# Kernel tuning notes

Measured on AMD Instinct MI355X. Metric: run time of the kernel, lower is better.

The kernel has to match this reference:

```python
import jax, jax.numpy as jnp
import numpy as np

H = 8
LN_EPS = 1e-5


def _layer_norm(t):
    # LayerNorm over last dim, no affine (elementwise_affine=False, bias=False)
    mu = jnp.mean(t, axis=-1, keepdims=True)
    var = jnp.var(t, axis=-1, keepdims=True)
    return (t - mu) / jnp.sqrt(var + LN_EPS)


def setup_inputs() -> dict:
    key = jax.random.key(0)
    ks = jax.random.split(key, 7)
    B, N, D, K = 2, 8192, 512, 32
    x = jax.random.normal(ks[0], (B, N, D), dtype=jnp.float32)
    idx = jax.random.randint(ks[1], (N, K), 0, N)
    s = 1.0 / np.sqrt(D)  # kaiming-ish init scale for stability
    Wq = jax.random.normal(ks[2], (D, D), dtype=jnp.float32) * s
    Wk = jax.random.normal(ks[3], (D, D), dtype=jnp.float32) * s
    Wv = jax.random.normal(ks[4], (D, D), dtype=jnp.float32) * s
    Wout = jax.random.normal(ks[5], (D, D), dtype=jnp.float32) * s
    bout = jnp.zeros((D,), dtype=jnp.float32)
    return {"x": x, "idx": idx, "Wq": Wq, "Wk": Wk, "Wv": Wv, "Wout": Wout, "bout": bout}


def reference(x, idx, Wq, Wk, Wv, Wout, bout):
    B, N, D = x.shape
    d_k = D // H

    def proj(W):
        # torch Linear: x @ W.T ; reshape to (B, H, N, d_k)
        return (x @ W.T).reshape(B, N, H, d_k).transpose(0, 2, 1, 3)

    Q, K, V = proj(Wq), proj(Wk), proj(Wv)
    # per-head LayerNorm on d_k (all heads identical since no affine params)
    Q = _layer_norm(Q)
    K = _layer_norm(K)

    # grouped (neighborhood) attention: gather K,V at neighbor indices
    Kg = K[:, :, idx]  # (B, H, N, k, d_k)
    Vg = V[:, :, idx]  # (B, H, N, k, d_k)
    scores = jnp.einsum('bhnd,bhnkd->bhnk', Q, Kg) / jnp.sqrt(jnp.asarray(d_k, x.dtype))
    attn = jax.nn.softmax(scores, axis=-1)
    out = jnp.einsum('bhnk,bhnkd->bhnd', attn, Vg)  # (B, H, N, d_k)

    out = out.transpose(0, 2, 1, 3).reshape(B, N, D)
    return out @ Wout.T + bout
```

## Files before the change

### kernel.cpp

```cpp
#include <hip/hip_runtime.h>
#include <hip/hip_bf16.h>
#include <math.h>

#define BB 2
#define NN 8192
#define DD 512
#define HH 8
#define DK 64
#define KNB 32
#define BN (BB*NN)
#define BHN (BB*HH*NN)

typedef __attribute__((ext_vector_type(8))) _Float16 f16x8;
typedef __attribute__((ext_vector_type(2))) _Float16 f16x2;
typedef __attribute__((ext_vector_type(4))) float f32x4;

#if __has_builtin(__builtin_amdgcn_fdot2)
#define HAS_FDOT2 1
#endif

__device__ __forceinline__ unsigned short f2h(float f) {
    return __builtin_bit_cast(unsigned short, (_Float16)f);
}
__device__ __forceinline__ f16x2 u2h2(unsigned u) {
    return __builtin_bit_cast(f16x2, u);
}
__device__ __forceinline__ float h2f_lo(unsigned u) {
    return (float)__builtin_bit_cast(_Float16, (unsigned short)(u & 0xffffu));
}
__device__ __forceinline__ float h2f_hi(unsigned u) {
    return (float)__builtin_bit_cast(_Float16, (unsigned short)(u >> 16));
}
__device__ __forceinline__ float dot2h(unsigned a, unsigned b, float c) {
#ifdef HAS_FDOT2
    return __builtin_amdgcn_fdot2(u2h2(a), u2h2(b), c, false);
#else
    c = fmaf(h2f_lo(a), h2f_lo(b), c);
    return fmaf(h2f_hi(a), h2f_hi(b), c);
#endif
}

__device__ __forceinline__ void gload_lds16(const void* gptr, void* lptr) {
    __builtin_amdgcn_global_load_lds(
        (const __attribute__((address_space(1))) unsigned int*)gptr,
        (__attribute__((address_space(3))) unsigned int*)lptr,
        16, 0, 0);
}

__global__ __launch_bounds__(256) void cvt_all(
    const float* __restrict__ x,
    const float* __restrict__ Wq, const float* __restrict__ Wk,
    const float* __restrict__ Wv, const float* __restrict__ Wo,
    unsigned short* __restrict__ Xb, unsigned short* __restrict__ Wfb,
    unsigned short* __restrict__ Wob)
{
    const int blk = blockIdx.x;
    const float* src;
    unsigned short* dst;
    int off;
    if (blk < 8192) {
        off = (blk * 256 + threadIdx.x) * 4;
        src = x; dst = Xb;
    } else {
        const int e = ((blk - 8192) * 256 + threadIdx.x) * 4;
        const int t = e >> 18;
        off = e & 262143;
        src = (t == 0) ? Wq : (t == 1) ? Wk : (t == 2) ? Wv : Wo;
        dst = (t < 3) ? (Wfb + (size_t)t * 262144) : Wob;
    }
    const float4 v = *(const float4*)(src + off);
    ushort4 u;
    u.x = f2h(v.x); u.y = f2h(v.y); u.z = f2h(v.z); u.w = f2h(v.w);
    *(ushort4*)(dst + off) = u;
}

__global__ __launch_bounds__(256) void gemm_qkv(
    const unsigned short* __restrict__ Xb, const unsigned short* __restrict__ Wfb,
    unsigned short* __restrict__ Qh, unsigned short* __restrict__ Kh,
    unsigned short* __restrict__ Vh)
{
    __shared__ unsigned short Als[2][128 * 32];
    __shared__ unsigned short Bls[2][128 * 32];
    const int tid  = threadIdx.x;
    const int wave = tid >> 6, lane = tid & 63;
    const int wm = wave >> 1, wn = wave & 1;
    const int quad = lane >> 4, r = lane & 15;
    const int p = blockIdx.x;
    const int L = (p & 7) * 192 + (p >> 3);
    const int row0 = (L / 12) * 128;
    const int c0   = (L % 12) * 128;

    f32x4 acc[4][4];
    #pragma unroll
    for (int i = 0; i < 4; ++i)
        #pragma unroll
        for (int j = 0; j < 4; ++j) acc[i][j] = (f32x4)0.f;

    const char* Ab = (const char*)Xb;
    const char* Bb = (const char*)Wfb;

    const int li0 = wave * 1024 + lane * 16;
    const int rr0 = li0 >> 6, off0 = li0 & 63;
    const int li1 = 4096 + li0;
    const int rr1 = li1 >> 6, off1 = li1 & 63;

    {
        gload_lds16(Ab + (size_t)(row0 + rr0) * 1024 + off0, (char*)Als[0] + (wave * 1024));
        gload_lds16(Bb + (size_t)(c0   + rr0) * 1024 + off0, (char*)Bls[0] + (wave * 1024));
        gload_lds16(Ab + (size_t)(row0 + rr1) * 1024 + off1, (char*)Als[0] + (4096 + wave * 1024));
        gload_lds16(Bb + (size_t)(c0   + rr1) * 1024 + off1, (char*)Bls[0] + (4096 + wave * 1024));
    }
    __syncthreads();

    for (int kt = 0; kt < 16; ++kt) {
        const int cur = kt & 1;
        if (kt < 15) {
            const int kb = (kt + 1) * 64;
            gload_lds16(Ab + (size_t)(row0 + rr0) * 1024 + kb + off0, (char*)Als[cur ^ 1] + (wave * 1024));
            gload_lds16(Bb + (size_t)(c0   + rr0) * 1024 + kb + off0, (char*)Bls[cur ^ 1] + (wave * 1024));
            gload_lds16(Ab + (size_t)(row0 + rr1) * 1024 + kb + off1, (char*)Als[cur ^ 1] + (4096 + wave * 1024));
            gload_lds16(Bb + (size_t)(c0   + rr1) * 1024 + kb + off1, (char*)Bls[cur ^ 1] + (4096 + wave * 1024));
        }

        f16x8 af[4], bf[4];
        #pragma unroll
        for (int i = 0; i < 4; ++i)
            af[i] = *(const f16x8*)(&Als[cur][(wm * 64 + i * 16 + r) * 32 + quad * 8]);
        #pragma unroll
        for (int j = 0; j < 4; ++j)
            bf[j] = *(const f16x8*)(&Bls[cur][(wn * 64 + j * 16 + r) * 32 + quad * 8]);
        #pragma unroll
        for (int i = 0; i < 4; ++i)
            #pragma unroll
            for (int j = 0; j < 4; ++j)
                acc[i][j] = __builtin_amdgcn_mfma_f32_16x16x32_f16(af[i], bf[j], acc[i][j], 0, 0, 0);

        __syncthreads();
    }

    const int tensor = c0 >> 9;
    unsigned short* OutH = (tensor == 0) ? Qh : (tensor == 1) ? Kh : Vh;

    float mu[4][4], rs[4][4];
    if (tensor < 2) {
        #pragma unroll
        for (int i = 0; i < 4; ++i) {
            #pragma unroll
            for (int reg = 0; reg < 4; ++reg) {
                float sm = acc[i][0][reg] + acc[i][1][reg] + acc[i][2][reg] + acc[i][3][reg];
                sm += __shfl_xor(sm, 1); sm += __shfl_xor(sm, 2);
                sm += __shfl_xor(sm, 4); sm += __shfl_xor(sm, 8);
                const float muv = sm * (1.f / 64.f);
                float qv = 0.f;
                #pragma unroll
                for (int j = 0; j < 4; ++j) {
                    const float dv = acc[i][j][reg] - muv;
                    qv = fmaf(dv, dv, qv);
                }
                qv += __shfl_xor(qv, 1); qv += __shfl_xor(qv, 2);
                qv += __shfl_xor(qv, 4); qv += __shfl_xor(qv, 8);
                mu[i][reg] = muv;
                rs[i][reg] = rsqrtf(qv * (1.f / 64.f) + 1e-5f);
            }
        }
    }

    #pragma unroll
    for (int i = 0; i < 4; ++i) {
        #pragma unroll
        for (int j = 0; j < 4; ++j) {
            const int cc = (c0 & 511) + wn * 64 + j * 16 + r;
            const int h = cc >> 6, d = cc & 63;
            #pragma unroll
            for (int reg = 0; reg < 4; ++reg) {
                const int row = row0 + wm * 64 + i * 16 + quad * 4 + reg;
                const int b = row >> 13, n = row & 8191;
                float v = acc[i][j][reg];
                if (tensor < 2) v = (v - mu[i][reg]) * rs[i][reg];
                OutH[(((size_t)(b * HH + h) * NN + n) << 6) + d] = f2h(v);
            }
        }
    }
}

__global__ __launch_bounds__(256, 2) void attn(
    const unsigned short* __restrict__ Qh, const unsigned short* __restrict__ Kh,
    const unsigned short* __restrict__ Vh,
    const int* __restrict__ idx, unsigned short* __restrict__ Ob)
{
    const int p = blockIdx.x;
    const int L = ((p & 7) << 12) | (p >> 3);
    const int wave = threadIdx.x >> 6;
    const int wid  = L * 4 + wave;
    const int lane = threadIdx.x & 63;
    const int bh = wid >> 13;
    const int n  = wid & 8191;
    const size_t base = (size_t)bh * NN * DK;

    const int g_all = idx[n * KNB + (lane & 31)];

    const int k    = lane >> 1;
    const int half = lane & 1;
    const int g    = __builtin_amdgcn_ds_bpermute(k * 4, g_all);

    const uint4* q4 = (const uint4*)(Qh + base + ((size_t)n << 6) + half * 32);
    const uint4* k4 = (const uint4*)(Kh + base + ((size_t)g << 6) + half * 32);
    float a0 = 0.f, a1 = 0.f;
    {
        const uint4 qa = q4[0], ka = k4[0];
        a0 = dot2h(qa.x, ka.x, a0); a0 = dot2h(qa.y, ka.y, a0);
        a0 = dot2h(qa.z, ka.z, a0); a0 = dot2h(qa.w, ka.w, a0);
    }
    {
        const uint4 qa = q4[1], ka = k4[1];
        a1 = dot2h(qa.x, ka.x, a1); a1 = dot2h(qa.y, ka.y, a1);
        a1 = dot2h(qa.z, ka.z, a1); a1 = dot2h(qa.w, ka.w, a1);
    }
    {
        const uint4 qa = q4[2], ka = k4[2];
        a0 = dot2h(qa.x, ka.x, a0); a0 = dot2h(qa.y, ka.y, a0);
        a0 = dot2h(qa.z, ka.z, a0); a0 = dot2h(qa.w, ka.w, a0);
    }
    {
        const uint4 qa = q4[3], ka = k4[3];
        a1 = dot2h(qa.x, ka.x, a1); a1 = dot2h(qa.y, ka.y, a1);
        a1 = dot2h(qa.z, ka.z, a1); a1 = dot2h(qa.w, ka.w, a1);
    }
    const float acc = a0 + a1;
    const float s = (acc + __shfl_xor(acc, 1)) * 0.125f;

    const float e = __expf(s);
    float tot = e;
    #pragma unroll
    for (int off = 2; off <= 32; off <<= 1) tot += __shfl_xor(tot, off);
    const float pr = e / tot;

    const unsigned prh = (unsigned)f2h(pr);
    const unsigned pp = prh | (((unsigned)__shfl_xor((int)prh, 2)) << 16);

    const char* Vbytes = (const char*)Vh + (base << 1);
    const int c2 = lane & 31, h2 = lane >> 5;
    float o0 = 0.f, o1 = 0.f;
    #pragma unroll
    for (int j = 0; j < 8; ++j) {
        const int r0 = __builtin_amdgcn_ds_bpermute((h2 * 16 + 2 * j) * 4, g_all);
        const int r1 = __builtin_amdgcn_ds_bpermute((h2 * 16 + 2 * j + 1) * 4, g_all);
        const unsigned vx = *(const unsigned*)(Vbytes + (size_t)(r0 * 128) + c2 * 4);
        const unsigned vy = *(const unsigned*)(Vbytes + (size_t)(r1 * 128) + c2 * 4);
        const unsigned ppj = (unsigned)__builtin_amdgcn_ds_bpermute(h2 * 128 + j * 16, (int)pp);
        const unsigned t0 = __builtin_amdgcn_perm(vx, vy, 0x01000504u);
        const unsigned t1 = __builtin_amdgcn_perm(vx, vy, 0x03020706u);
        o0 = dot2h(t0, ppj, o0);
        o1 = dot2h(t1, ppj, o1);
    }
    o0 += __shfl_xor(o0, 32);
    o1 += __shfl_xor(o1, 32);
    if (lane < 32) {
        const int b = bh >> 3, hh = bh & 7;
        const unsigned ov = (unsigned)f2h(o0) | ((unsigned)f2h(o1) << 16);
        *(unsigned*)(Ob + ((size_t)(b * NN + n)) * DD + hh * DK + 2 * c2) = ov;
    }
}

__global__ __launch_bounds__(256) void gemm_out(
    const unsigned short* __restrict__ Ob, const unsigned short* __restrict__ Wob,
    const float* __restrict__ bout, float* __restrict__ out)
{
    __shared__ unsigned short Als[2][128 * 32];
    __shared__ unsigned short Bls[2][128 * 32];
    const int tid  = threadIdx.x;
    const int wave = tid >> 6, lane = tid & 63;
    const int wm = wave >> 1, wn = wave & 1;
    const int quad = lane >> 4, r = lane & 15;
    const int p = blockIdx.x;
    const int L = (p & 7) * 64 + (p >> 3);
    const int row0 = (L >> 2) * 128;
    const int c0   = (L & 3) * 128;

    f32x4 acc[4][4];
    #pragma unroll
    for (int i = 0; i < 4; ++i)
        #pragma unroll
        for (int j = 0; j < 4; ++j) acc[i][j] = (f32x4)0.f;

    const char* Ab = (const char*)Ob;
    const char* Bb = (const char*)Wob;

    const int li0 = wave * 1024 + lane * 16;
    const int rr0 = li0 >> 6, off0 = li0 & 63;
    const int li1 = 4096 + li0;
    const int rr1 = li1 >> 6, off1 = li1 & 63;

    {
        gload_lds16(Ab + (size_t)(row0 + rr0) * 1024 + off0, (char*)Als[0] + (wave * 1024));
        gload_lds16(Bb + (size_t)(c0   + rr0) * 1024 + off0, (char*)Bls[0] + (wave * 1024));
        gload_lds16(Ab + (size_t)(row0 + rr1) * 1024 + off1, (char*)Als[0] + (4096 + wave * 1024));
        gload_lds16(Bb + (size_t)(c0   + rr1) * 1024 + off1, (char*)Bls[0] + (4096 + wave * 1024));
    }
    __syncthreads();

    for (int kt = 0; kt < 16; ++kt) {
        const int cur = kt & 1;
        if (kt < 15) {
            const int kb = (kt + 1) * 64;
            gload_lds16(Ab + (size_t)(row0 + rr0) * 1024 + kb + off0, (char*)Als[cur ^ 1] + (wave * 1024));
            gload_lds16(Bb + (size_t)(c0   + rr0) * 1024 + kb + off0, (char*)Bls[cur ^ 1] + (wave * 1024));
            gload_lds16(Ab + (size_t)(row0 + rr1) * 1024 + kb + off1, (char*)Als[cur ^ 1] + (4096 + wave * 1024));
            gload_lds16(Bb + (size_t)(c0   + rr1) * 1024 + kb + off1, (char*)Bls[cur ^ 1] + (4096 + wave * 1024));
        }

        f16x8 af[4], bf[4];
        #pragma unroll
        for (int i = 0; i < 4; ++i)
            af[i] = *(const f16x8*)(&Als[cur][(wm * 64 + i * 16 + r) * 32 + quad * 8]);
        #pragma unroll
        for (int j = 0; j < 4; ++j)
            bf[j] = *(const f16x8*)(&Bls[cur][(wn * 64 + j * 16 + r) * 32 + quad * 8]);
        #pragma unroll
        for (int i = 0; i < 4; ++i)
            #pragma unroll
            for (int j = 0; j < 4; ++j)
                acc[i][j] = __builtin_amdgcn_mfma_f32_16x16x32_f16(af[i], bf[j], acc[i][j], 0, 0, 0);

        __syncthreads();
    }

    #pragma unroll
    for (int i = 0; i < 4; ++i) {
        #pragma unroll
        for (int j = 0; j < 4; ++j) {
            const int colg = c0 + wn * 64 + j * 16 + r;
            const float bb = bout[colg];
            #pragma unroll
            for (int reg = 0; reg < 4; ++reg) {
                const int row = row0 + wm * 64 + i * 16 + quad * 4 + reg;
                out[((size_t)row << 9) + colg] = acc[i][j][reg] + bb;
            }
        }
    }
}

extern "C" void kernel_launch(void* const* d_in, const int* in_sizes, int n_in,
                              void* d_out, int out_size, void* d_ws, size_t ws_size,
                              hipStream_t stream)
{
    const float* x    = (const float*)d_in[0];
    const int*   idx  = (const int*)  d_in[1];
    const float* Wq   = (const float*)d_in[2];
    const float* Wk   = (const float*)d_in[3];
    const float* Wv   = (const float*)d_in[4];
    const float* Wout = (const float*)d_in[5];
    const float* bout = (const float*)d_in[6];

    char* ws = (char*)d_ws;
    unsigned short* Qh  = (unsigned short*)(ws);
    unsigned short* Kh  = (unsigned short*)(ws + 16777216);
    unsigned short* Vh  = (unsigned short*)(ws + 33554432);
    unsigned short* Xb  = (unsigned short*)(ws + 50331648);
    unsigned short* Ob  = Xb;
    unsigned short* Wfb = (unsigned short*)(ws + 67108864);
    unsigned short* Wob = (unsigned short*)(ws + 68681728);
    float* out = (float*)d_out;

    cvt_all<<<9216, 256, 0, stream>>>(x, Wq, Wk, Wv, Wout, Xb, Wfb, Wob);

    gemm_qkv<<<1536, 256, 0, stream>>>(Xb, Wfb, Qh, Kh, Vh);

    attn<<<BHN / 4, 256, 0, stream>>>(Qh, Kh, Vh, idx, Ob);

    gemm_out<<<512, 256, 0, stream>>>(Ob, Wob, bout, out);
}
```

Baseline: 221.2 us.

## Fuse fp32-to-fp16 conversion of x into the QKV GEMM A-tile load

Removes the separate conversion pass over x. The QKV GEMM now loads fp32 x tiles into registers, converts them to packed fp16 with cvt_pkrtz, and writes them to LDS after the MFMA work for the current tile. The weight-only conversion kernel remains. This saves a 16 MB fp32 read plus an 8 MB fp16 write and its readback. In exchange, the GEMM reads twice as many A bytes from global memory, and each x row is reread by all 12 column blocks, through cache. Conversion also changes from default rounding to round-toward-zero.

```diff
diff --git a/kernel.cpp b/kernel.cpp
--- a/kernel.cpp
+++ b/kernel.cpp
@@ -40,6 +40,10 @@
 #endif
 }
 
+__device__ __forceinline__ unsigned cvt2h(float lo, float hi) {
+    return __builtin_bit_cast(unsigned, __builtin_amdgcn_cvt_pkrtz(lo, hi));
+}
+
 __device__ __forceinline__ void gload_lds16(const void* gptr, void* lptr) {
     __builtin_amdgcn_global_load_lds(
         (const __attribute__((address_space(1))) unsigned int*)gptr,
@@ -47,27 +51,16 @@
         16, 0, 0);
 }
 
-__global__ __launch_bounds__(256) void cvt_all(
-    const float* __restrict__ x,
+__global__ __launch_bounds__(256) void cvt_w(
     const float* __restrict__ Wq, const float* __restrict__ Wk,
     const float* __restrict__ Wv, const float* __restrict__ Wo,
-    unsigned short* __restrict__ Xb, unsigned short* __restrict__ Wfb,
-    unsigned short* __restrict__ Wob)
-{
-    const int blk = blockIdx.x;
-    const float* src;
-    unsigned short* dst;
-    int off;
-    if (blk < 8192) {
-        off = (blk * 256 + threadIdx.x) * 4;
-        src = x; dst = Xb;
-    } else {
-        const int e = ((blk - 8192) * 256 + threadIdx.x) * 4;
-        const int t = e >> 18;
-        off = e & 262143;
-        src = (t == 0) ? Wq : (t == 1) ? Wk : (t == 2) ? Wv : Wo;
-        dst = (t < 3) ? (Wfb + (size_t)t * 262144) : Wob;
-    }
+    unsigned short* __restrict__ Wfb, unsigned short* __restrict__ Wob)
+{
+    const int e = (blockIdx.x * 256 + threadIdx.x) * 4;
+    const int t = e >> 18;
+    const int off = e & 262143;
+    const float* src = (t == 0) ? Wq : (t == 1) ? Wk : (t == 2) ? Wv : Wo;
+    unsigned short* dst = (t < 3) ? (Wfb + (size_t)t * 262144) : Wob;
     const float4 v = *(const float4*)(src + off);
     ushort4 u;
     u.x = f2h(v.x); u.y = f2h(v.y); u.z = f2h(v.z); u.w = f2h(v.w);
@@ -75,7 +68,7 @@
 }
 
 __global__ __launch_bounds__(256) void gemm_qkv(
-    const unsigned short* __restrict__ Xb, const unsigned short* __restrict__ Wfb,
+    const float* __restrict__ x, const unsigned short* __restrict__ Wfb,
     unsigned short* __restrict__ Qh, unsigned short* __restrict__ Kh,
     unsigned short* __restrict__ Vh)
 {
@@ -96,7 +89,6 @@
         #pragma unroll
         for (int j = 0; j < 4; ++j) acc[i][j] = (f32x4)0.f;
 
-    const char* Ab = (const char*)Xb;
     const char* Bb = (const char*)Wfb;
 
     const int li0 = wave * 1024 + lane * 16;
@@ -104,22 +96,34 @@
     const int li1 = 4096 + li0;
     const int rr1 = li1 >> 6, off1 = li1 & 63;
 
-    {
-        gload_lds16(Ab + (size_t)(row0 + rr0) * 1024 + off0, (char*)Als[0] + (wave * 1024));
-        gload_lds16(Bb + (size_t)(c0   + rr0) * 1024 + off0, (char*)Bls[0] + (wave * 1024));
-        gload_lds16(Ab + (size_t)(row0 + rr1) * 1024 + off1, (char*)Als[0] + (4096 + wave * 1024));
-        gload_lds16(Bb + (size_t)(c0   + rr1) * 1024 + off1, (char*)Bls[0] + (4096 + wave * 1024));
+    const int ar = tid >> 3;
+    const int aq = tid & 7;
+
+    float4 va[4];
+    #pragma unroll
+    for (int i = 0; i < 4; ++i)
+        va[i] = *(const float4*)(x + (size_t)(row0 + i * 32 + ar) * 512 + aq * 4);
+    gload_lds16(Bb + (size_t)(c0 + rr0) * 1024 + off0, (char*)Bls[0] + (wave * 1024));
+    gload_lds16(Bb + (size_t)(c0 + rr1) * 1024 + off1, (char*)Bls[0] + (4096 + wave * 1024));
+    #pragma unroll
+    for (int i = 0; i < 4; ++i) {
+        uint2 u;
+        u.x = cvt2h(va[i].x, va[i].y);
+        u.y = cvt2h(va[i].z, va[i].w);
+        *(uint2*)((char*)Als[0] + (i * 32 + ar) * 64 + aq * 8) = u;
     }
     __syncthreads();
 
     for (int kt = 0; kt < 16; ++kt) {
         const int cur = kt & 1;
         if (kt < 15) {
+            const int ke = (kt + 1) * 32;
+            #pragma unroll
+            for (int i = 0; i < 4; ++i)
+                va[i] = *(const float4*)(x + (size_t)(row0 + i * 32 + ar) * 512 + ke + aq * 4);
             const int kb = (kt + 1) * 64;
-            gload_lds16(Ab + (size_t)(row0 + rr0) * 1024 + kb + off0, (char*)Als[cur ^ 1] + (wave * 1024));
-            gload_lds16(Bb + (size_t)(c0   + rr0) * 1024 + kb + off0, (char*)Bls[cur ^ 1] + (wave * 1024));
-            gload_lds16(Ab + (size_t)(row0 + rr1) * 1024 + kb + off1, (char*)Als[cur ^ 1] + (4096 + wave * 1024));
-            gload_lds16(Bb + (size_t)(c0   + rr1) * 1024 + kb + off1, (char*)Bls[cur ^ 1] + (4096 + wave * 1024));
+            gload_lds16(Bb + (size_t)(c0 + rr0) * 1024 + kb + off0, (char*)Bls[cur ^ 1] + (wave * 1024));
+            gload_lds16(Bb + (size_t)(c0 + rr1) * 1024 + kb + off1, (char*)Bls[cur ^ 1] + (4096 + wave * 1024));
         }
 
         f16x8 af[4], bf[4];
@@ -135,6 +139,15 @@
             for (int j = 0; j < 4; ++j)
                 acc[i][j] = __builtin_amdgcn_mfma_f32_16x16x32_f16(af[i], bf[j], acc[i][j], 0, 0, 0);
 
+        if (kt < 15) {
+            #pragma unroll
+            for (int i = 0; i < 4; ++i) {
+                uint2 u;
+                u.x = cvt2h(va[i].x, va[i].y);
+                u.y = cvt2h(va[i].z, va[i].w);
+                *(uint2*)((char*)Als[cur ^ 1] + (i * 32 + ar) * 64 + aq * 8) = u;
+            }
+        }
         __syncthreads();
     }
 
@@ -356,15 +369,14 @@
     unsigned short* Qh  = (unsigned short*)(ws);
     unsigned short* Kh  = (unsigned short*)(ws + 16777216);
     unsigned short* Vh  = (unsigned short*)(ws + 33554432);
-    unsigned short* Xb  = (unsigned short*)(ws + 50331648);
-    unsigned short* Ob  = Xb;
+    unsigned short* Ob  = (unsigned short*)(ws + 50331648);
     unsigned short* Wfb = (unsigned short*)(ws + 67108864);
     unsigned short* Wob = (unsigned short*)(ws + 68681728);
     float* out = (float*)d_out;
 
-    cvt_all<<<9216, 256, 0, stream>>>(x, Wq, Wk, Wv, Wout, Xb, Wfb, Wob);
-
-    gemm_qkv<<<1536, 256, 0, stream>>>(Xb, Wfb, Qh, Kh, Vh);
+    cvt_w<<<1024, 256, 0, stream>>>(Wq, Wk, Wv, Wout, Wfb, Wob);
+
+    gemm_qkv<<<1536, 256, 0, stream>>>(x, Wfb, Qh, Kh, Vh);
 
     attn<<<BHN / 4, 256, 0, stream>>>(Qh, Kh, Vh, idx, Ob);
 
```

New measurement: 235.3 us. +6.4%, slower.
